# Kernel optimization log

Hardware: AMD Instinct MI355X
Metric: run time of the kernel (lower is better)

The kernel has to match this reference:

```python
import jax, jax.numpy as jnp
import numpy as np

H = 8          # heads
F = 256        # hidden dim (hid_dim_1 == hid_dim_2)
D = F // H     # per-head dim = 32
NE = 3         # num edge types
NT = 2         # num node types: 0=op, 1=var
N = 50000      # nodes per type
E = 150000     # edges per edge type
F3 = 128       # hid_dim_3 = hid_dim_2 // 2
C = 16         # out_channels
ETYPES = [(0, 1), (1, 0), (0, 0)]  # (src_type, dst_type) per edge type
SQRT_D = float(np.sqrt(D))


def gelu(x):
    return jax.nn.gelu(x, approximate=False)  # torch F.gelu default (erf)


def layer_norm(x, g, b):
    mu = jnp.mean(x, -1, keepdims=True)
    var = jnp.mean((x - mu) ** 2, -1, keepdims=True)
    return (x - mu) * jax.lax.rsqrt(var + 1e-5) * g + b


def segment_softmax(a, seg, num_segments):
    # PyG softmax: subtract per-segment max, add 1e-16 to denominator
    m = jax.ops.segment_max(a, seg, num_segments=num_segments)
    m = jnp.where(jnp.isfinite(m), m, 0.0)
    e = jnp.exp(a - m[seg])
    s = jax.ops.segment_sum(e, seg, num_segments=num_segments)
    return e / (s[seg] + 1e-16)


def hgt_conv(xs, eis, Wkqv, bkqv, Wkrel, Wvrel, prel, Wout, bout, skip):
    # fused per-node-type K/Q/V projection, split as torch.tensor_split(., 3, dim=1)
    kqv = [xs[t] @ Wkqv[t] + bkqv[t] for t in range(NT)]
    k = [a[:, :F].reshape(-1, H, D) for a in kqv]
    q = [a[:, F:2 * F].reshape(-1, H, D) for a in kqv]
    v = [a[:, 2 * F:].reshape(-1, H, D) for a in kqv]
    off = [0]
    for x in xs:
        off.append(off[-1] + x.shape[0])
    ntot = off[-1]
    alphas, vjs, dsts = [], [], []
    for e, (st, dt) in enumerate(ETYPES):
        # per-(head, edge-type) relation transforms of source K/V (k_rel / v_rel)
        ke = jnp.einsum('nhd,hde->nhe', k[st], Wkrel[:, e])
        ve = jnp.einsum('nhd,hde->nhe', v[st], Wvrel[:, e])
        src, dst = eis[e][0], eis[e][1]
        a = jnp.sum(q[dt][dst] * ke[src], -1) * prel[e] / SQRT_D  # [E, H]
        alphas.append(a)
        vjs.append(ve[src])
        dsts.append(dst + off[dt])
    seg = jnp.concatenate(dsts, 0)
    # softmax over ALL incoming edges of a dst node across edge types (bipartite union)
    a = segment_softmax(jnp.concatenate(alphas, 0), seg, ntot)
    agg = jax.ops.segment_sum(jnp.concatenate(vjs, 0) * a[:, :, None], seg,
                              num_segments=ntot).reshape(ntot, F)
    outs = []
    for t in range(NT):
        o = gelu(agg[off[t]:off[t + 1]]) @ Wout[t] + bout[t]
        s = jax.nn.sigmoid(skip[t])
        outs.append(s * o + (1.0 - s) * xs[t])  # in==out -> skip gate active
    return outs


def _forward(x_op, x_var,
             l1_Wkqv, l1_bkqv, l1_Wkrel, l1_Wvrel, l1_prel, l1_Wout, l1_bout, l1_skip,
             l2_Wkqv, l2_bkqv, l2_Wkrel, l2_Wvrel, l2_prel, l2_Wout, l2_bout, l2_skip,
             l3_Wkqv, l3_bkqv, l3_Wkrel, l3_Wvrel, l3_prel, l3_Wout, l3_bout, l3_skip,
             ln_g, ln_b, Wagg1, bagg1, Wagg2, bagg2, Wo, bo,
             ei_ov, ei_vo, ei_oo):
    xs = [x_op, x_var]
    eis = [ei_ov, ei_vo, ei_oo]
    h = hgt_conv(xs, eis, l1_Wkqv, l1_bkqv, l1_Wkrel, l1_Wvrel, l1_prel, l1_Wout, l1_bout, l1_skip)
    h = [gelu(layer_norm(h[t], ln_g[t], ln_b[t])) for t in range(NT)]  # dropout = identity (eval)
    h = hgt_conv(h, eis, l2_Wkqv, l2_bkqv, l2_Wkrel, l2_Wvrel, l2_prel, l2_Wout, l2_bout, l2_skip)
    h = [gelu(x) for x in h]
    h = hgt_conv(h, eis, l3_Wkqv, l3_bkqv, l3_Wkrel, l3_Wvrel, l3_prel, l3_Wout, l3_bout, l3_skip)
    h = [gelu(x) for x in h]
    # HeteroLinear lin_agg_1 with type_vec = node type id (sorted by construction)
    ha = jnp.concatenate([h[0] @ Wagg1[0] + bagg1[0],
                          h[1] @ Wagg1[1] + bagg1[1]], 0)
    ha = jnp.mean(gelu(ha), 0)          # mean over all nodes -> [F]
    ha = gelu(ha @ Wagg2 + bagg2)       # [F3]
    return jnp.nan_to_num(ha @ Wo + bo) # [C]


def setup_inputs():
    key = jax.random.key(0)
    ks = jax.random.split(key, 64)
    it = iter(range(64))
    def nrm(shape, scale=0.05):
        return jax.random.normal(ks[next(it)], shape, dtype=jnp.float32) * scale
    inp = {
        'x_op': nrm((N, F), 1.0),
        'x_var': nrm((N, F), 1.0),
    }
    for i in (1, 2, 3):
        inp[f'l{i}_Wkqv'] = nrm((NT, F, 3 * F))
        inp[f'l{i}_bkqv'] = jnp.zeros((NT, 3 * F), jnp.float32)
        inp[f'l{i}_Wkrel'] = nrm((H, NE, D, D), 0.15)
        inp[f'l{i}_Wvrel'] = nrm((H, NE, D, D), 0.15)
        inp[f'l{i}_prel'] = jnp.ones((NE, H), jnp.float32)
        inp[f'l{i}_Wout'] = nrm((NT, F, F))
        inp[f'l{i}_bout'] = jnp.zeros((NT, F), jnp.float32)
        inp[f'l{i}_skip'] = jnp.ones((NT,), jnp.float32)
    inp['ln_g'] = jnp.ones((NT, F), jnp.float32)
    inp['ln_b'] = jnp.zeros((NT, F), jnp.float32)
    inp['Wagg1'] = nrm((NE, F, F))
    inp['bagg1'] = jnp.zeros((NE, F), jnp.float32)
    inp['Wagg2'] = nrm((F, F3))
    inp['bagg2'] = jnp.zeros((F3,), jnp.float32)
    inp['Wo'] = nrm((F3, C))
    inp['bo'] = jnp.zeros((C,), jnp.float32)
    ek = jax.random.split(jax.random.key(1), 3)
    inp['ei_ov'] = jax.random.randint(ek[0], (2, E), 0, N, dtype=jnp.int32)
    inp['ei_vo'] = jax.random.randint(ek[1], (2, E), 0, N, dtype=jnp.int32)
    inp['ei_oo'] = jax.random.randint(ek[2], (2, E), 0, N, dtype=jnp.int32)
    return inp


def reference(x_op, x_var,
              l1_Wkqv, l1_bkqv, l1_Wkrel, l1_Wvrel, l1_prel, l1_Wout, l1_bout, l1_skip,
              l2_Wkqv, l2_bkqv, l2_Wkrel, l2_Wvrel, l2_prel, l2_Wout, l2_bout, l2_skip,
              l3_Wkqv, l3_bkqv, l3_Wkrel, l3_Wvrel, l3_prel, l3_Wout, l3_bout, l3_skip,
              ln_g, ln_b, Wagg1, bagg1, Wagg2, bagg2, Wo, bo,
              ei_ov, ei_vo, ei_oo):
    return _forward(x_op, x_var,
                    l1_Wkqv, l1_bkqv, l1_Wkrel, l1_Wvrel, l1_prel, l1_Wout, l1_bout, l1_skip,
                    l2_Wkqv, l2_bkqv, l2_Wkrel, l2_Wvrel, l2_prel, l2_Wout, l2_bout, l2_skip,
                    l3_Wkqv, l3_bkqv, l3_Wkrel, l3_Wvrel, l3_prel, l3_Wout, l3_bout, l3_skip,
                    ln_g, ln_b, Wagg1, bagg1, Wagg2, bagg2, Wo, bo,
                    ei_ov, ei_vo, ei_oo)
```

## Files before the change

### kernel.cpp

```cpp
#include <hip/hip_runtime.h>
#include <math.h>

#define NN   50000
#define NTOT 100000
#define FD   256
#define EC   150000
#define NCH  98

static const size_t NF = (size_t)NN * FD;

typedef __attribute__((ext_vector_type(8))) short bf16x8;
typedef __attribute__((ext_vector_type(4))) float f32x4;

__device__ __forceinline__ float gelu_f(float x) {
  return 0.5f * x * (1.0f + erff(x * 0.7071067811865475f));
}
__device__ __forceinline__ unsigned short f2bf(float x) {
  unsigned u = __float_as_uint(x);
  u += 0x7FFFu + ((u >> 16) & 1u);
  return (unsigned short)(u >> 16);
}
__device__ __forceinline__ float bf2f(unsigned short u) {
  return __uint_as_float((unsigned)u << 16);
}

template<int MODE, int XSF>
__global__ __launch_bounds__(256) void gemm_bf(
    const unsigned short* __restrict__ A,
    const unsigned short* __restrict__ Bt,
    const float* __restrict__ bias,
    void* d0, void* d1, void* d2,
    const void* Xs, const float* __restrict__ skipp, int M)
{
  __shared__ unsigned short As[128 * 64];
  __shared__ unsigned short Bs[128 * 64];
  const int tid = threadIdx.x;
  const int lane = tid & 63;
  const int wave = tid >> 6;
  const int wr = wave >> 1, wc = wave & 1;
  const int l15 = lane & 15, lq = lane >> 4;
  const int bm = blockIdx.y * 128, bn = blockIdx.x * 128;
  const int sr = tid >> 1, sg0 = (tid & 1) * 4;
  const bool av = (bm + sr) < M;
  const unsigned short* ag = A  + (size_t)(bm + sr) * 256 + sg0 * 8;
  const unsigned short* bg = Bt + (size_t)(bn + sr) * 256 + sg0 * 8;

  f32x4 acc[4][4] = {};
  uint4 ra[4], rb[4];

#define LOADT(KT) { \
    const unsigned short* ap = ag + (KT) * 64; \
    const unsigned short* bp = bg + (KT) * 64; \
    if (av) { ra[0] = *(const uint4*)(ap);      ra[1] = *(const uint4*)(ap + 8); \
              ra[2] = *(const uint4*)(ap + 16); ra[3] = *(const uint4*)(ap + 24); } \
    else    { ra[0] = ra[1] = ra[2] = ra[3] = make_uint4(0,0,0,0); } \
    rb[0] = *(const uint4*)(bp);      rb[1] = *(const uint4*)(bp + 8); \
    rb[2] = *(const uint4*)(bp + 16); rb[3] = *(const uint4*)(bp + 24); }

  LOADT(0);
  for (int kt = 0; kt < 4; kt++) {
    __syncthreads();
    #pragma unroll
    for (int i = 0; i < 4; i++) {
      const int g = sg0 + i;
      *(uint4*)&As[sr * 64 + ((g ^ (sr & 7)) << 3)] = ra[i];
      *(uint4*)&Bs[sr * 64 + ((g ^ (sr & 7)) << 3)] = rb[i];
    }
    __syncthreads();
    if (kt < 3) LOADT(kt + 1);
    #pragma unroll
    for (int ks = 0; ks < 2; ks++) {
      bf16x8 af[4], bv[4];
      const int g = ks * 4 + lq;
      #pragma unroll
      for (int mi = 0; mi < 4; mi++) {
        const int r = wr * 64 + mi * 16 + l15;
        af[mi] = *(const bf16x8*)&As[r * 64 + ((g ^ (r & 7)) << 3)];
      }
      #pragma unroll
      for (int ni = 0; ni < 4; ni++) {
        const int c = wc * 64 + ni * 16 + l15;
        bv[ni] = *(const bf16x8*)&Bs[c * 64 + ((g ^ (c & 7)) << 3)];
      }
      #pragma unroll
      for (int mi = 0; mi < 4; mi++)
        #pragma unroll
        for (int ni = 0; ni < 4; ni++)
          acc[mi][ni] = __builtin_amdgcn_mfma_f32_16x16x32_bf16(
              af[mi], bv[ni], acc[mi][ni], 0, 0, 0);
    }
  }
#undef LOADT

  const int seg = (MODE == 0 || MODE == 3) ? (bn >> 8) : 0;
  float sg = 0.f;
  if (MODE == 1) sg = 1.f / (1.f + expf(-skipp[0]));
  #pragma unroll
  for (int mi = 0; mi < 4; mi++) {
    #pragma unroll
    for (int ni = 0; ni < 4; ni++) {
      const int cp = bn + wc * 64 + ni * 16 + l15;
      const float bc_ = bias[cp];
      const int co = (MODE == 0 || MODE == 3) ? (cp & 255) : cp;
      #pragma unroll
      for (int j = 0; j < 4; j++) {
        const int r = bm + wr * 64 + mi * 16 + lq * 4 + j;
        if (r >= M) continue;
        float v = acc[mi][ni][j] + bc_;
        const size_t oidx = (size_t)r * 256 + co;
        if (MODE == 2) {
          ((float*)d0)[oidx] = gelu_f(v);
        } else if (MODE == 1) {
          const float xs = XSF ? bf2f(((const unsigned short*)Xs)[oidx])
                               : ((const float*)Xs)[oidx];
          ((unsigned short*)d0)[oidx] = f2bf(sg * v + (1.f - sg) * xs);
        } else if (MODE == 0) {
          if (seg == 0) ((float*)d0)[oidx] = v;
          else ((unsigned short*)(seg == 1 ? d1 : d2))[oidx] = f2bf(v);
        } else {
          ((unsigned short*)(seg == 0 ? d0 : d1))[oidx] = f2bf(v);
        }
      }
    }
  }
}

__global__ __launch_bounds__(256) void wcomb_kernel(
    const float* __restrict__ Wkqv, const float* __restrict__ bkqv,
    const float* __restrict__ Wkrel, const float* __restrict__ Wvrel,
    const float* __restrict__ prel,
    unsigned short* __restrict__ Bo1t, unsigned short* __restrict__ Bvt,
    unsigned short* __restrict__ Bo3t,
    float* __restrict__ bias_o1, float* __restrict__ bias_v, float* __restrict__ bias_o3)
{
  const int z = blockIdx.x, et = z >> 1, kv = z & 1;
  const int h = blockIdx.y;
  const int st = (et == 1) ? 1 : 0;
  const int cbase = (kv ? 512 : 0) + h * 32;
  const float scale = kv ? 1.0f : (prel[et*8 + h] * 0.1767766952966369f);
  unsigned short* Bdst; int ofs; float* bdst;
  if (z == 0)      { Bdst = Bo1t; ofs = 0;   bdst = bias_o1; }
  else if (z == 1) { Bdst = Bo1t; ofs = 256; bdst = bias_o1; }
  else if (z == 2) { Bdst = Bvt;  ofs = 256; bdst = bias_v;  }
  else if (z == 3) { Bdst = Bvt;  ofs = 512; bdst = bias_v;  }
  else if (z == 4) { Bdst = Bo3t; ofs = 256; bdst = bias_o3; }
  else             { Bdst = Bo3t; ofs = 512; bdst = bias_o3; }
  __shared__ float Wr[32][32];
  const int tid = threadIdx.x;
  {
    const float* wr = (kv ? Wvrel : Wkrel) + ((size_t)(h*3 + et)) * 1024;
    for (int i = tid; i < 1024; i += 256) Wr[i >> 5][i & 31] = wr[i];
  }
  __syncthreads();
  const float* w1 = Wkqv + (size_t)st * 196608 + (size_t)tid * 768 + cbase;
  float acc[32] = {};
  for (int d = 0; d < 32; d++) {
    float v = w1[d];
    #pragma unroll
    for (int j = 0; j < 32; j++) acc[j] = fmaf(v, Wr[d][j], acc[j]);
  }
  for (int j = 0; j < 32; j++)
    Bdst[(size_t)(ofs + h * 32 + j) * 256 + tid] = f2bf(acc[j] * scale);
  if (tid < 32) {
    const float* bk = bkqv + st * 768 + cbase;
    float a = 0.f;
    for (int d = 0; d < 32; d++) a = fmaf(bk[d], Wr[d][tid], a);
    bdst[ofs + h * 32 + tid] = a * scale;
  }
}

__global__ __launch_bounds__(256) void qpack_kernel(
    const float* __restrict__ Wkqv, const float* __restrict__ bkqv,
    unsigned short* __restrict__ Bo3t, unsigned short* __restrict__ Bvt,
    float* __restrict__ bias_o3, float* __restrict__ bias_v)
{
  const int t = blockIdx.y;
  const int bx = blockIdx.x & 7, by = blockIdx.x >> 3;
  const int tx = threadIdx.x & 31, ty = threadIdx.x >> 5;
  __shared__ float tile[32][33];
  #pragma unroll
  for (int k = 0; k < 4; k++) {
    int r = by*32 + ty + 8*k, c = bx*32 + tx;
    tile[ty + 8*k][tx] = Wkqv[(size_t)t*196608 + (size_t)r*768 + 256 + c];
  }
  __syncthreads();
  unsigned short* dst = t ? Bvt : Bo3t;
  #pragma unroll
  for (int k = 0; k < 4; k++) {
    int c = bx*32 + ty + 8*k, r = by*32 + tx;
    dst[(size_t)c*256 + r] = f2bf(tile[tx][ty + 8*k]);
  }
  if (blockIdx.x == 0) {
    (t ? bias_v : bias_o3)[threadIdx.x] = bkqv[t*768 + 256 + threadIdx.x];
  }
}

__global__ __launch_bounds__(256) void wcvt_kernel(
    const float* __restrict__ src, unsigned short* __restrict__ dst)
{
  const int bx = blockIdx.x & 7, by = blockIdx.x >> 3;
  const int tx = threadIdx.x & 31, ty = threadIdx.x >> 5;
  __shared__ float tile[32][33];
  #pragma unroll
  for (int k = 0; k < 4; k++)
    tile[ty + 8*k][tx] = src[(size_t)(by*32 + ty + 8*k)*256 + bx*32 + tx];
  __syncthreads();
  #pragma unroll
  for (int k = 0; k < 4; k++)
    dst[(size_t)(bx*32 + ty + 8*k)*256 + by*32 + tx] = f2bf(tile[tx][ty + 8*k]);
}

__global__ __launch_bounds__(256) void attn_union(
    const float* __restrict__ qb,
    const unsigned short* __restrict__ KEu,
    const unsigned short* __restrict__ VEu,
    const int* __restrict__ indptr, const int* __restrict__ adj,
    unsigned short* __restrict__ aggb)
{
  const int wid = (int)(((size_t)blockIdx.x * 256 + threadIdx.x) >> 6);
  if (wid >= NN) return;
  const int lane = threadIdx.x & 63;
  const int off = lane * 4;
  const float4 q4 = *(const float4*)(qb + (size_t)wid * FD + off);
  float m = -INFINITY, s = 0.f, ax = 0.f, ay = 0.f, az = 0.f, aw = 0.f;
  const int beg = indptr[wid], end = indptr[wid + 1];
  for (int i = beg; i < end; i++) {
    const int src = adj[i];
    ushort4 ku = *(const ushort4*)(KEu + (size_t)src * FD + off);
    float d = q4.x*bf2f(ku.x) + q4.y*bf2f(ku.y) + q4.z*bf2f(ku.z) + q4.w*bf2f(ku.w);
    d += __shfl_xor(d, 1); d += __shfl_xor(d, 2); d += __shfl_xor(d, 4);
    float mn = fmaxf(m, d);
    float sc = expf(m - mn);
    float w  = expf(d - mn);
    s = s * sc + w;
    ushort4 vu = *(const ushort4*)(VEu + (size_t)src * FD + off);
    ax = ax*sc + w*bf2f(vu.x); ay = ay*sc + w*bf2f(vu.y);
    az = az*sc + w*bf2f(vu.z); aw = aw*sc + w*bf2f(vu.w);
    m = mn;
  }
  const float inv = 1.f / (s + 1e-16f);
  ushort4 o;
  o.x = f2bf(gelu_f(ax * inv)); o.y = f2bf(gelu_f(ay * inv));
  o.z = f2bf(gelu_f(az * inv)); o.w = f2bf(gelu_f(aw * inv));
  *(ushort4*)(aggb + (size_t)wid * FD + off) = o;
}

__global__ __launch_bounds__(256) void ln_gelu_kernel(
    unsigned short* __restrict__ x, const float* __restrict__ g,
    const float* __restrict__ b)
{
  const int wid = (int)(((size_t)blockIdx.x * 256 + threadIdx.x) >> 6);
  if (wid >= NTOT) return;
  const int lane = threadIdx.x & 63;
  const int t = (wid >= NN) ? 1 : 0;
  ushort4 u = *(ushort4*)(x + (size_t)wid * FD + lane*4);
  float vx = bf2f(u.x), vy = bf2f(u.y), vz = bf2f(u.z), vw = bf2f(u.w);
  float sum = vx + vy + vz + vw;
  #pragma unroll
  for (int o = 1; o < 64; o <<= 1) sum += __shfl_xor(sum, o);
  float mu = sum * (1.f/256.f);
  float dx = vx-mu, dy = vy-mu, dz = vz-mu, dw = vw-mu;
  float vs = dx*dx + dy*dy + dz*dz + dw*dw;
  #pragma unroll
  for (int o = 1; o < 64; o <<= 1) vs += __shfl_xor(vs, o);
  float var = vs * (1.f/256.f);
  float rs = 1.f / sqrtf(var + 1e-5f);
  int c = lane*4;
  float4 gv = *(const float4*)(g + t*FD + c);
  float4 bv = *(const float4*)(b + t*FD + c);
  ushort4 o4;
  o4.x = f2bf(gelu_f(dx*rs*gv.x + bv.x));
  o4.y = f2bf(gelu_f(dy*rs*gv.y + bv.y));
  o4.z = f2bf(gelu_f(dz*rs*gv.z + bv.z));
  o4.w = f2bf(gelu_f(dw*rs*gv.w + bv.w));
  *(ushort4*)(x + (size_t)wid * FD + c) = o4;
}

__global__ __launch_bounds__(256) void gelu_bf_kernel(
    unsigned short* __restrict__ x, size_t n4)
{
  size_t i = ((size_t)blockIdx.x * 256 + threadIdx.x);
  if (i >= n4) return;
  ushort4 u = ((ushort4*)x)[i];
  u.x = f2bf(gelu_f(bf2f(u.x))); u.y = f2bf(gelu_f(bf2f(u.y)));
  u.z = f2bf(gelu_f(bf2f(u.z))); u.w = f2bf(gelu_f(bf2f(u.w)));
  ((ushort4*)x)[i] = u;
}

__global__ __launch_bounds__(256) void cvt_bf_kernel(
    const float* __restrict__ src, unsigned short* __restrict__ dst, size_t n4)
{
  size_t i = ((size_t)blockIdx.x * 256 + threadIdx.x);
  if (i >= n4) return;
  float4 v = ((const float4*)src)[i];
  ushort4 o; o.x = f2bf(v.x); o.y = f2bf(v.y); o.z = f2bf(v.z); o.w = f2bf(v.w);
  ((ushort4*)dst)[i] = o;
}

__global__ __launch_bounds__(256) void count_v(const int* __restrict__ e0,
                                               int* __restrict__ degv) {
  int i = blockIdx.x * 256 + threadIdx.x;
  if (i >= EC) return;
  atomicAdd(&degv[e0[EC + i]], 1);
}
__global__ __launch_bounds__(256) void count_o(const int* __restrict__ e1,
                                               const int* __restrict__ e2,
                                               int* __restrict__ dego) {
  int i = blockIdx.x * 256 + threadIdx.x;
  if (i >= 2*EC) return;
  int dst = (i < EC) ? e1[EC + i] : e2[EC + (i - EC)];
  atomicAdd(&dego[dst], 1);
}

__global__ __launch_bounds__(256) void scan_part(
    const int* __restrict__ deg,
    int* __restrict__ psum)
{
  const int arr = blockIdx.y, ch = blockIdx.x, tid = threadIdx.x;
  int i0 = ch*512 + tid, i1 = i0 + 256;
  int s = ((i0 < NN) ? deg[arr*NN + i0] : 0) + ((i1 < NN) ? deg[arr*NN + i1] : 0);
  __shared__ int red[256];
  red[tid] = s; __syncthreads();
  #pragma unroll
  for (int off = 128; off > 0; off >>= 1) {
    if (tid < off) red[tid] += red[tid + off];
    __syncthreads();
  }
  if (tid == 0) psum[arr*NCH + ch] = red[0];
}

__global__ __launch_bounds__(256) void scan_mid(int* __restrict__ psum)
{
  const int tid = threadIdx.x;
  __shared__ int buf[2*NCH];
  if (tid < 2*NCH) buf[tid] = psum[tid];
  __syncthreads();
  if (tid < 2) {
    int run = 0;
    for (int i = 0; i < NCH; i++) { int t = buf[tid*NCH + i]; buf[tid*NCH + i] = run; run += t; }
  }
  __syncthreads();
  if (tid < 2*NCH) psum[tid] = buf[tid];
}

__global__ __launch_bounds__(256) void scan_fin(
    const int* __restrict__ deg, const int* __restrict__ psum,
    int* __restrict__ ipv, int* __restrict__ ipo,
    int* __restrict__ cv, int* __restrict__ co)
{
  const int arr = blockIdx.y, ch = blockIdx.x, tid = threadIdx.x;
  __shared__ int buf[512];
  __shared__ int s2[256];
  int i0 = ch*512 + 2*tid, i1 = i0 + 1;
  buf[2*tid]   = (i0 < NN) ? deg[arr*NN + i0] : 0;
  buf[2*tid+1] = (i1 < NN) ? deg[arr*NN + i1] : 0;
  __syncthreads();
  s2[tid] = buf[2*tid] + buf[2*tid+1];
  __syncthreads();
  #pragma unroll
  for (int off = 1; off < 256; off <<= 1) {
    int v = (tid >= off) ? s2[tid - off] : 0;
    __syncthreads();
    s2[tid] += v;
    __syncthreads();
  }
  int ex = (tid ? s2[tid - 1] : 0) + psum[arr*NCH + ch];
  int e0 = ex, e1 = ex + buf[2*tid];
  int* ip  = arr ? ipo : ipv;
  int* cur = arr ? co  : cv;
  if (i0 < NN) { ip[i0] = e0; cur[i0] = e0; }
  if (i1 < NN) { ip[i1] = e1; cur[i1] = e1; }
  if (ch == 0 && tid == 0) ip[NN] = arr ? 2*EC : EC;
}

__global__ __launch_bounds__(256) void scat_v(const int* __restrict__ e0,
                                              int* __restrict__ cv,
                                              int* __restrict__ adjv) {
  int i = blockIdx.x * 256 + threadIdx.x;
  if (i >= EC) return;
  int pos = atomicAdd(&cv[e0[EC + i]], 1);
  adjv[pos] = e0[i];
}
__global__ __launch_bounds__(256) void scat_o(const int* __restrict__ e1,
                                              const int* __restrict__ e2,
                                              int* __restrict__ co,
                                              int* __restrict__ adjo) {
  int i = blockIdx.x * 256 + threadIdx.x;
  if (i >= 2*EC) return;
  int dst, srcg;
  if (i < EC) { dst = e1[EC + i]; srcg = NN + e1[i]; }
  else        { int j = i - EC; dst = e2[EC + j]; srcg = e2[j]; }
  int pos = atomicAdd(&co[dst], 1);
  adjo[pos] = srcg;
}

__global__ __launch_bounds__(256) void colmean_kernel(
    const float* __restrict__ gmat, double* __restrict__ outp, int n)
{
  const int c = threadIdx.x;
  const int r0 = blockIdx.x * 256;
  int rend = r0 + 256; if (rend > n) rend = n;
  double sum = 0.0;
  for (int r = r0; r < rend; r++) sum += (double)gmat[(size_t)r * FD + c];
  atomicAdd(&outp[c], sum);
}

__global__ __launch_bounds__(256) void head_kernel(
    const double* __restrict__ meand,
    const float* __restrict__ Wagg2, const float* __restrict__ bagg2,
    const float* __restrict__ Wo, const float* __restrict__ bo,
    float* __restrict__ outp)
{
  __shared__ float mv[256];
  __shared__ float h2[128];
  const int tid = threadIdx.x;
  mv[tid] = (float)(meand[tid] * (1.0 / (double)NTOT));
  __syncthreads();
  if (tid < 128) {
    float acc = bagg2[tid];
    for (int k = 0; k < 256; k++) acc = fmaf(mv[k], Wagg2[k*128 + tid], acc);
    h2[tid] = gelu_f(acc);
  }
  __syncthreads();
  if (tid < 16) {
    float acc = bo[tid];
    for (int k = 0; k < 128; k++) acc = fmaf(h2[k], Wo[k*16 + tid], acc);
    if (isnan(acc)) acc = 0.f;
    else if (isinf(acc)) acc = (acc > 0.f) ? 3.4028234663852886e38f : -3.4028234663852886e38f;
    outp[tid] = acc;
  }
}

__global__ void fill_kernel(float* p, int n, float v) {
  int i = blockIdx.x * 64 + threadIdx.x;
  if (i < n) p[i] = v;
}

extern "C" void kernel_launch(void* const* d_in, const int* in_sizes, int n_in,
                              void* d_out, int out_size, void* d_ws, size_t ws_size,
                              hipStream_t stream)
{
  const float* x_op_in  = (const float*)d_in[0];
  const float* x_var_in = (const float*)d_in[1];
  struct LayerP { const float *Wkqv,*bkqv,*Wkrel,*Wvrel,*prel,*Wout,*bout,*skip; };
  LayerP L[3];
  for (int i = 0; i < 3; i++) {
    int b = 2 + i*8;
    L[i].Wkqv  = (const float*)d_in[b+0];
    L[i].bkqv  = (const float*)d_in[b+1];
    L[i].Wkrel = (const float*)d_in[b+2];
    L[i].Wvrel = (const float*)d_in[b+3];
    L[i].prel  = (const float*)d_in[b+4];
    L[i].Wout  = (const float*)d_in[b+5];
    L[i].bout  = (const float*)d_in[b+6];
    L[i].skip  = (const float*)d_in[b+7];
  }
  const float* ln_g  = (const float*)d_in[26];
  const float* ln_b  = (const float*)d_in[27];
  const float* Wagg1 = (const float*)d_in[28];
  const float* bagg1 = (const float*)d_in[29];
  const float* Wagg2 = (const float*)d_in[30];
  const float* bagg2 = (const float*)d_in[31];
  const float* Wo    = (const float*)d_in[32];
  const float* bo    = (const float*)d_in[33];
  const int* e0 = (const int*)d_in[34];
  const int* e1 = (const int*)d_in[35];
  const int* e2 = (const int*)d_in[36];

  float* base = (float*)d_ws;
  unsigned short* Xb   = (unsigned short*)base;
  unsigned short* Xbop = Xb;
  unsigned short* Xbvar= Xb + NF;
  float* Qb            = base + NF;
  unsigned short* aggb = (unsigned short*)(base + 2*NF);
  unsigned short* KEu  = (unsigned short*)(base + 2*NF + NF/2);
  unsigned short* VEu  = (unsigned short*)(base + 3*NF + NF/2);
  float* wb            = base + 4*NF + NF/2;
  unsigned short* Bo1t = (unsigned short*)wb;
  unsigned short* Bvt  = Bo1t + 512*256;
  unsigned short* Bo3t = Bvt + 768*256;
  unsigned short* Wtt  = Bo3t + 768*256;
  float* b_o1 = (float*)(Wtt + 8*65536);
  float* b_v  = b_o1 + 512;
  float* b_o3 = b_v + 768;
  double* meand = (double*)(b_o3 + 768);
  int* ipv  = (int*)(meand + 256);
  int* ipo  = ipv + (NN + 1);
  int* cv   = ipo + (NN + 1);
  int* co   = cv + NN;
  int* degv = co + NN;
  int* dego = degv + NN;
  int* adjv = dego + NN;
  int* adjo = adjv + EC;
  int* psum = adjo + 2*EC;
  size_t need = (size_t)((char*)(psum + 2*NCH) - (char*)d_ws);
  if (ws_size < need) {
    float v = (float)(ws_size >> 20) * 1000.0f;
    fill_kernel<<<dim3((out_size + 63)/64), 64, 0, stream>>>((float*)d_out, out_size, v);
    return;
  }

  hipMemsetAsync(degv, 0, 2*NN*sizeof(int), stream);
  hipMemsetAsync(meand, 0, 256*sizeof(double), stream);
  count_v<<<dim3((EC + 255)/256), 256, 0, stream>>>(e0, degv);
  count_o<<<dim3((2*EC + 255)/256), 256, 0, stream>>>(e1, e2, dego);
  scan_part<<<dim3(NCH, 2), 256, 0, stream>>>(degv, psum);
  scan_mid<<<dim3(1), 256, 0, stream>>>(psum);
  scan_fin<<<dim3(NCH, 2), 256, 0, stream>>>(degv, psum, ipv, ipo, cv, co);
  scat_v<<<dim3((EC + 255)/256), 256, 0, stream>>>(e0, cv, adjv);
  scat_o<<<dim3((2*EC + 255)/256), 256, 0, stream>>>(e1, e2, co, adjo);

  for (int i = 0; i < 3; i++) {
    wcvt_kernel<<<dim3(64), 256, 0, stream>>>(L[i].Wout,         Wtt + (size_t)(i*2)  *65536);
    wcvt_kernel<<<dim3(64), 256, 0, stream>>>(L[i].Wout + 65536, Wtt + (size_t)(i*2+1)*65536);
  }
  wcvt_kernel<<<dim3(64), 256, 0, stream>>>(Wagg1,         Wtt + (size_t)6*65536);
  wcvt_kernel<<<dim3(64), 256, 0, stream>>>(Wagg1 + 65536, Wtt + (size_t)7*65536);
  cvt_bf_kernel<<<dim3((int)(NF/4 + 255)/256), 256, 0, stream>>>(x_op_in,  Xbop,  NF/4);
  cvt_bf_kernel<<<dim3((int)(NF/4 + 255)/256), 256, 0, stream>>>(x_var_in, Xbvar, NF/4);

  const dim3 gw6(6, 391), gw4(4, 391), gw2(2, 391);
  const dim3 ga((NN*64 + 255)/256);

  for (int layer = 0; layer < 3; layer++) {
    const LayerP& P = L[layer];
    const unsigned short* Wo_op  = Wtt + (size_t)(layer*2)  *65536;
    const unsigned short* Wo_var = Wtt + (size_t)(layer*2+1)*65536;

    wcomb_kernel<<<dim3(6, 8), 256, 0, stream>>>(P.Wkqv, P.bkqv, P.Wkrel, P.Wvrel,
                                                 P.prel, Bo1t, Bvt, Bo3t, b_o1, b_v, b_o3);
    qpack_kernel<<<dim3(64, 2), 256, 0, stream>>>(P.Wkqv, P.bkqv, Bo3t, Bvt, b_o3, b_v);

    gemm_bf<3,0><<<gw4, 256, 0, stream>>>(
        Xbop, Bo1t, b_o1, KEu, VEu, nullptr, nullptr, nullptr, NN);
    gemm_bf<0,0><<<gw6, 256, 0, stream>>>(
        Xbvar, Bvt, b_v, Qb, KEu + NF, VEu + NF, nullptr, nullptr, NN);
    attn_union<<<ga, 256, 0, stream>>>(Qb, KEu, VEu, ipv, adjv, aggb);
    if (layer == 0)
      gemm_bf<1,0><<<gw2, 256, 0, stream>>>(aggb, Wo_var, P.bout + 256,
          Xbvar, nullptr, nullptr, x_var_in, P.skip + 1, NN);
    else
      gemm_bf<1,1><<<gw2, 256, 0, stream>>>(aggb, Wo_var, P.bout + 256,
          Xbvar, nullptr, nullptr, Xbvar, P.skip + 1, NN);

    gemm_bf<0,0><<<gw6, 256, 0, stream>>>(
        Xbop, Bo3t, b_o3, Qb, KEu, VEu, nullptr, nullptr, NN);
    attn_union<<<ga, 256, 0, stream>>>(Qb, KEu, VEu, ipo, adjo, aggb);
    if (layer == 0)
      gemm_bf<1,0><<<gw2, 256, 0, stream>>>(aggb, Wo_op, P.bout,
          Xbop, nullptr, nullptr, x_op_in, P.skip, NN);
    else
      gemm_bf<1,1><<<gw2, 256, 0, stream>>>(aggb, Wo_op, P.bout,
          Xbop, nullptr, nullptr, Xbop, P.skip, NN);

    if (layer == 0)
      ln_gelu_kernel<<<dim3((NTOT*64 + 255)/256), 256, 0, stream>>>(Xb, ln_g, ln_b);
    else
      gelu_bf_kernel<<<dim3((int)(2*NF/4 + 255)/256), 256, 0, stream>>>(Xb, 2*NF/4);
  }

  gemm_bf<2,0><<<gw2, 256, 0, stream>>>(Xbop, Wtt + (size_t)6*65536, bagg1,
      Qb, nullptr, nullptr, nullptr, nullptr, NN);
  colmean_kernel<<<dim3((NN + 255)/256), 256, 0, stream>>>(Qb, meand, NN);
  gemm_bf<2,0><<<gw2, 256, 0, stream>>>(Xbvar, Wtt + (size_t)7*65536, bagg1 + 256,
      Qb, nullptr, nullptr, nullptr, nullptr, NN);
  colmean_kernel<<<dim3((NN + 255)/256), 256, 0, stream>>>(Qb, meand, NN);
  head_kernel<<<dim3(1), 256, 0, stream>>>(meand, Wagg2, bagg2, Wo, bo, (float*)d_out);
}
```

Baseline: 2.097 ms.

## Stage GEMM epilogue through LDS, store Q in bf16, fuse GELU, XCD-aware tiles

```diff
diff --git a/kernel.cpp b/kernel.cpp
--- a/kernel.cpp
+++ b/kernel.cpp
@@ -24,7 +24,12 @@
   return __uint_as_float((unsigned)u << 16);
 }
 
-template<int MODE, int XSF>
+__device__ __forceinline__ int ep_gaddr(int row, int g) {
+  int gs = (g & 8) | ((g ^ (row & 7)) & 7);
+  return row * 128 + gs * 8;
+}
+
+template<int MODE, int XSF, int GC, int NBN>
 __global__ __launch_bounds__(256) void gemm_bf(
     const unsigned short* __restrict__ A,
     const unsigned short* __restrict__ Bt,
@@ -32,14 +37,20 @@
     void* d0, void* d1, void* d2,
     const void* Xs, const float* __restrict__ skipp, int M)
 {
-  __shared__ unsigned short As[128 * 64];
-  __shared__ unsigned short Bs[128 * 64];
+  __shared__ unsigned short SB[2 * 128 * 64];
+  unsigned short* As = SB;
+  unsigned short* Bs = SB + 128 * 64;
   const int tid = threadIdx.x;
   const int lane = tid & 63;
   const int wave = tid >> 6;
   const int wr = wave >> 1, wc = wave & 1;
   const int l15 = lane & 15, lq = lane >> 4;
-  const int bm = blockIdx.y * 128, bn = blockIdx.x * 128;
+  const int nwg = NBN * 391;
+  const int orig = blockIdx.x;
+  const int qq = nwg >> 3, rr8 = nwg & 7;
+  const int xcd = orig & 7, loc = orig >> 3;
+  const int wg = (xcd < rr8 ? xcd * (qq + 1) : rr8 * (qq + 1) + (xcd - rr8) * qq) + loc;
+  const int bm = (wg / NBN) * 128, bn = (wg % NBN) * 128;
   const int sr = tid >> 1, sg0 = (tid & 1) * 4;
   const bool av = (bm + sr) < M;
   const unsigned short* ag = A  + (size_t)(bm + sr) * 256 + sg0 * 8;
@@ -92,35 +103,71 @@
   }
 #undef LOADT
 
-  const int seg = (MODE == 0 || MODE == 3) ? (bn >> 8) : 0;
-  float sg = 0.f;
-  if (MODE == 1) sg = 1.f / (1.f + expf(-skipp[0]));
+  __syncthreads();
   #pragma unroll
   for (int mi = 0; mi < 4; mi++) {
     #pragma unroll
     for (int ni = 0; ni < 4; ni++) {
-      const int cp = bn + wc * 64 + ni * 16 + l15;
-      const float bc_ = bias[cp];
-      const int co = (MODE == 0 || MODE == 3) ? (cp & 255) : cp;
+      const int col = wc * 64 + ni * 16 + l15;
+      const float bc_ = bias[bn + col];
+      const int g = col >> 3;
       #pragma unroll
       for (int j = 0; j < 4; j++) {
-        const int r = bm + wr * 64 + mi * 16 + lq * 4 + j;
-        if (r >= M) continue;
+        const int row = wr * 64 + mi * 16 + lq * 4 + j;
         float v = acc[mi][ni][j] + bc_;
-        const size_t oidx = (size_t)r * 256 + co;
-        if (MODE == 2) {
-          ((float*)d0)[oidx] = gelu_f(v);
-        } else if (MODE == 1) {
-          const float xs = XSF ? bf2f(((const unsigned short*)Xs)[oidx])
-                               : ((const float*)Xs)[oidx];
-          ((unsigned short*)d0)[oidx] = f2bf(sg * v + (1.f - sg) * xs);
-        } else if (MODE == 0) {
-          if (seg == 0) ((float*)d0)[oidx] = v;
-          else ((unsigned short*)(seg == 1 ? d1 : d2))[oidx] = f2bf(v);
+        if (MODE == 2) v = gelu_f(v);
+        SB[ep_gaddr(row, g) + (col & 7)] = f2bf(v);
+      }
+    }
+  }
+  __syncthreads();
+
+  const int seg = (MODE == 0 || MODE == 3) ? (bn >> 8) : 0;
+  const int cb  = (MODE == 0 || MODE == 3) ? (bn & 255) : bn;
+  unsigned short* dst;
+  if (MODE == 0)      dst = (unsigned short*)(seg == 0 ? d0 : (seg == 1 ? d1 : d2));
+  else if (MODE == 3) dst = (unsigned short*)(seg == 0 ? d0 : d1);
+  else                dst = (unsigned short*)d0;
+  float sg = 0.f;
+  if (MODE == 1) sg = 1.f / (1.f + expf(-skipp[0]));
+  const int rt = tid >> 1, half = tid & 1;
+  const int r = bm + rt;
+  if (r < M) {
+    #pragma unroll
+    for (int k = 0; k < 8; k++) {
+      const int colbase = half * 64 + k * 8;
+      const int g = colbase >> 3;
+      uint4 w = *(const uint4*)&SB[ep_gaddr(rt, g)];
+      if (MODE == 1) {
+        const size_t xi = (size_t)r * 256 + cb + colbase;
+        float xv[8];
+        if (XSF) {
+          uint4 xu = *(const uint4*)&((const unsigned short*)Xs)[xi];
+          xv[0]=bf2f(xu.x&0xffff); xv[1]=bf2f(xu.x>>16);
+          xv[2]=bf2f(xu.y&0xffff); xv[3]=bf2f(xu.y>>16);
+          xv[4]=bf2f(xu.z&0xffff); xv[5]=bf2f(xu.z>>16);
+          xv[6]=bf2f(xu.w&0xffff); xv[7]=bf2f(xu.w>>16);
         } else {
-          ((unsigned short*)(seg == 0 ? d0 : d1))[oidx] = f2bf(v);
+          float4 x0 = *(const float4*)&((const float*)Xs)[xi];
+          float4 x1 = *(const float4*)&((const float*)Xs)[xi + 4];
+          xv[0]=x0.x; xv[1]=x0.y; xv[2]=x0.z; xv[3]=x0.w;
+          xv[4]=x1.x; xv[5]=x1.y; xv[6]=x1.z; xv[7]=x1.w;
         }
+        unsigned e[8] = { w.x&0xffffu, w.x>>16, w.y&0xffffu, w.y>>16,
+                          w.z&0xffffu, w.z>>16, w.w&0xffffu, w.w>>16 };
+        unsigned short o[8];
+        #pragma unroll
+        for (int i = 0; i < 8; i++) {
+          float v = sg * bf2f((unsigned short)e[i]) + (1.f - sg) * xv[i];
+          if (GC) v = gelu_f(v);
+          o[i] = f2bf(v);
+        }
+        w.x = o[0] | ((unsigned)o[1] << 16);
+        w.y = o[2] | ((unsigned)o[3] << 16);
+        w.z = o[4] | ((unsigned)o[5] << 16);
+        w.w = o[6] | ((unsigned)o[7] << 16);
       }
+      *(uint4*)&dst[(size_t)r * 256 + cb + colbase] = w;
     }
   }
 }
@@ -211,7 +258,7 @@
 }
 
 __global__ __launch_bounds__(256) void attn_union(
-    const float* __restrict__ qb,
+    const unsigned short* __restrict__ qb,
     const unsigned short* __restrict__ KEu,
     const unsigned short* __restrict__ VEu,
     const int* __restrict__ indptr, const int* __restrict__ adj,
@@ -221,13 +268,14 @@
   if (wid >= NN) return;
   const int lane = threadIdx.x & 63;
   const int off = lane * 4;
-  const float4 q4 = *(const float4*)(qb + (size_t)wid * FD + off);
+  ushort4 qu = *(const ushort4*)(qb + (size_t)wid * FD + off);
+  const float qx = bf2f(qu.x), qy = bf2f(qu.y), qz = bf2f(qu.z), qw = bf2f(qu.w);
   float m = -INFINITY, s = 0.f, ax = 0.f, ay = 0.f, az = 0.f, aw = 0.f;
   const int beg = indptr[wid], end = indptr[wid + 1];
   for (int i = beg; i < end; i++) {
     const int src = adj[i];
     ushort4 ku = *(const ushort4*)(KEu + (size_t)src * FD + off);
-    float d = q4.x*bf2f(ku.x) + q4.y*bf2f(ku.y) + q4.z*bf2f(ku.z) + q4.w*bf2f(ku.w);
+    float d = qx*bf2f(ku.x) + qy*bf2f(ku.y) + qz*bf2f(ku.z) + qw*bf2f(ku.w);
     d += __shfl_xor(d, 1); d += __shfl_xor(d, 2); d += __shfl_xor(d, 4);
     float mn = fmaxf(m, d);
     float sc = expf(m - mn);
@@ -276,17 +324,6 @@
   *(ushort4*)(x + (size_t)wid * FD + c) = o4;
 }
 
-__global__ __launch_bounds__(256) void gelu_bf_kernel(
-    unsigned short* __restrict__ x, size_t n4)
-{
-  size_t i = ((size_t)blockIdx.x * 256 + threadIdx.x);
-  if (i >= n4) return;
-  ushort4 u = ((ushort4*)x)[i];
-  u.x = f2bf(gelu_f(bf2f(u.x))); u.y = f2bf(gelu_f(bf2f(u.y)));
-  u.z = f2bf(gelu_f(bf2f(u.z))); u.w = f2bf(gelu_f(bf2f(u.w)));
-  ((ushort4*)x)[i] = u;
-}
-
 __global__ __launch_bounds__(256) void cvt_bf_kernel(
     const float* __restrict__ src, unsigned short* __restrict__ dst, size_t n4)
 {
@@ -313,8 +350,7 @@
 }
 
 __global__ __launch_bounds__(256) void scan_part(
-    const int* __restrict__ deg,
-    int* __restrict__ psum)
+    const int* __restrict__ deg, int* __restrict__ psum)
 {
   const int arr = blockIdx.y, ch = blockIdx.x, tid = threadIdx.x;
   int i0 = ch*512 + tid, i1 = i0 + 256;
@@ -395,13 +431,13 @@
 }
 
 __global__ __launch_bounds__(256) void colmean_kernel(
-    const float* __restrict__ gmat, double* __restrict__ outp, int n)
+    const unsigned short* __restrict__ gmat, double* __restrict__ outp, int n)
 {
   const int c = threadIdx.x;
   const int r0 = blockIdx.x * 256;
   int rend = r0 + 256; if (rend > n) rend = n;
   double sum = 0.0;
-  for (int r = r0; r < rend; r++) sum += (double)gmat[(size_t)r * FD + c];
+  for (int r = r0; r < rend; r++) sum += (double)bf2f(gmat[(size_t)r * FD + c]);
   atomicAdd(&outp[c], sum);
 }
 
@@ -471,7 +507,7 @@
   unsigned short* Xb   = (unsigned short*)base;
   unsigned short* Xbop = Xb;
   unsigned short* Xbvar= Xb + NF;
-  float* Qb            = base + NF;
+  unsigned short* Qbf  = (unsigned short*)(base + NF);
   unsigned short* aggb = (unsigned short*)(base + 2*NF);
   unsigned short* KEu  = (unsigned short*)(base + 2*NF + NF/2);
   unsigned short* VEu  = (unsigned short*)(base + 3*NF + NF/2);
@@ -519,7 +555,7 @@
   cvt_bf_kernel<<<dim3((int)(NF/4 + 255)/256), 256, 0, stream>>>(x_op_in,  Xbop,  NF/4);
   cvt_bf_kernel<<<dim3((int)(NF/4 + 255)/256), 256, 0, stream>>>(x_var_in, Xbvar, NF/4);
 
-  const dim3 gw6(6, 391), gw4(4, 391), gw2(2, 391);
+  const dim3 gw6(6*391), gw4(4*391), gw2(2*391);
   const dim3 ga((NN*64 + 255)/256);
 
   for (int layer = 0; layer < 3; layer++) {
@@ -531,39 +567,37 @@
                                                  P.prel, Bo1t, Bvt, Bo3t, b_o1, b_v, b_o3);
     qpack_kernel<<<dim3(64, 2), 256, 0, stream>>>(P.Wkqv, P.bkqv, Bo3t, Bvt, b_o3, b_v);
 
-    gemm_bf<3,0><<<gw4, 256, 0, stream>>>(
+    gemm_bf<3,0,0,4><<<gw4, 256, 0, stream>>>(
         Xbop, Bo1t, b_o1, KEu, VEu, nullptr, nullptr, nullptr, NN);
-    gemm_bf<0,0><<<gw6, 256, 0, stream>>>(
-        Xbvar, Bvt, b_v, Qb, KEu + NF, VEu + NF, nullptr, nullptr, NN);
-    attn_union<<<ga, 256, 0, stream>>>(Qb, KEu, VEu, ipv, adjv, aggb);
+    gemm_bf<0,0,0,6><<<gw6, 256, 0, stream>>>(
+        Xbvar, Bvt, b_v, Qbf, KEu + NF, VEu + NF, nullptr, nullptr, NN);
+    attn_union<<<ga, 256, 0, stream>>>(Qbf, KEu, VEu, ipv, adjv, aggb);
     if (layer == 0)
-      gemm_bf<1,0><<<gw2, 256, 0, stream>>>(aggb, Wo_var, P.bout + 256,
+      gemm_bf<1,0,0,2><<<gw2, 256, 0, stream>>>(aggb, Wo_var, P.bout + 256,
           Xbvar, nullptr, nullptr, x_var_in, P.skip + 1, NN);
     else
-      gemm_bf<1,1><<<gw2, 256, 0, stream>>>(aggb, Wo_var, P.bout + 256,
+      gemm_bf<1,1,1,2><<<gw2, 256, 0, stream>>>(aggb, Wo_var, P.bout + 256,
           Xbvar, nullptr, nullptr, Xbvar, P.skip + 1, NN);
 
-    gemm_bf<0,0><<<gw6, 256, 0, stream>>>(
-        Xbop, Bo3t, b_o3, Qb, KEu, VEu, nullptr, nullptr, NN);
-    attn_union<<<ga, 256, 0, stream>>>(Qb, KEu, VEu, ipo, adjo, aggb);
+    gemm_bf<0,0,0,6><<<gw6, 256, 0, stream>>>(
+        Xbop, Bo3t, b_o3, Qbf, KEu, VEu, nullptr, nullptr, NN);
+    attn_union<<<ga, 256, 0, stream>>>(Qbf, KEu, VEu, ipo, adjo, aggb);
     if (layer == 0)
-      gemm_bf<1,0><<<gw2, 256, 0, stream>>>(aggb, Wo_op, P.bout,
+      gemm_bf<1,0,0,2><<<gw2, 256, 0, stream>>>(aggb, Wo_op, P.bout,
           Xbop, nullptr, nullptr, x_op_in, P.skip, NN);
     else
-      gemm_bf<1,1><<<gw2, 256, 0, stream>>>(aggb, Wo_op, P.bout,
+      gemm_bf<1,1,1,2><<<gw2, 256, 0, stream>>>(aggb, Wo_op, P.bout,
           Xbop, nullptr, nullptr, Xbop, P.skip, NN);
 
     if (layer == 0)
       ln_gelu_kernel<<<dim3((NTOT*64 + 255)/256), 256, 0, stream>>>(Xb, ln_g, ln_b);
-    else
-      gelu_bf_kernel<<<dim3((int)(2*NF/4 + 255)/256), 256, 0, stream>>>(Xb, 2*NF/4);
-  }
-
-  gemm_bf<2,0><<<gw2, 256, 0, stream>>>(Xbop, Wtt + (size_t)6*65536, bagg1,
-      Qb, nullptr, nullptr, nullptr, nullptr, NN);
-  colmean_kernel<<<dim3((NN + 255)/256), 256, 0, stream>>>(Qb, meand, NN);
-  gemm_bf<2,0><<<gw2, 256, 0, stream>>>(Xbvar, Wtt + (size_t)7*65536, bagg1 + 256,
-      Qb, nullptr, nullptr, nullptr, nullptr, NN);
-  colmean_kernel<<<dim3((NN + 255)/256), 256, 0, stream>>>(Qb, meand, NN);
+  }
+
+  gemm_bf<2,0,0,2><<<gw2, 256, 0, stream>>>(Xbop, Wtt + (size_t)6*65536, bagg1,
+      Qbf, nullptr, nullptr, nullptr, nullptr, NN);
+  colmean_kernel<<<dim3((NN + 255)/256), 256, 0, stream>>>(Qbf, meand, NN);
+  gemm_bf<2,0,0,2><<<gw2, 256, 0, stream>>>(Xbvar, Wtt + (size_t)7*65536, bagg1 + 256,
+      Qbf, nullptr, nullptr, nullptr, nullptr, NN);
+  colmean_kernel<<<dim3((NN + 255)/256), 256, 0, stream>>>(Qbf, meand, NN);
   head_kernel<<<dim3(1), 256, 0, stream>>>(meand, Wagg2, bagg2, Wo, bo, (float*)d_out);
 }
```

New measurement: 1.854 ms. 11.6% less time.
